# Kernel tuning notes

Hardware: AMD Instinct MI355X
Metric: run time of the kernel (lower is better)

Reference implementation:

```python
import jax, jax.numpy as jnp
import numpy as np

B, S, D, H = 2, 2048, 1024, 16
HEAD_DIM = D // H  # 64


def setup_inputs() -> dict:
    key = jax.random.key(0)
    ks = jax.random.split(key, 7)
    x = jax.random.normal(ks[0], (B, S, D), dtype=jnp.float32)
    W_q = jax.random.normal(ks[1], (D, D), dtype=jnp.float32) * 0.02
    W_k = jax.random.normal(ks[2], (D, D), dtype=jnp.float32) * 0.02
    W_v = jax.random.normal(ks[3], (D, D), dtype=jnp.float32) * 0.02
    W_o = jax.random.normal(ks[4], (D, D), dtype=jnp.float32) * 0.02 / np.sqrt(2 * 12)
    b_o = jnp.zeros((D,), dtype=jnp.float32)
    # Ragged prefix attention_mask: per-row valid lengths in [S/2, S];
    # row 0 forced to full length so max_valid_len == S statically (jit-safe).
    lengths = jax.random.randint(ks[5], (B,), S // 2, S + 1)
    lengths = lengths.at[0].set(S)
    attention_mask = (jnp.arange(S)[None, :] < lengths[:, None]).astype(jnp.float32)
    return {"x": x, "attention_mask": attention_mask, "W_q": W_q, "W_k": W_k,
            "W_v": W_v, "W_o": W_o, "b_o": b_o}


def reference(x, attention_mask, W_q, W_k, W_v, W_o, b_o):
    b, s, d = x.shape
    h, hd = H, HEAD_DIM
    # QKV projections (no bias, qkv_bias=False)
    q = (x @ W_q.T).reshape(b, s, h, hd).transpose(0, 2, 1, 3)  # [b,h,s,hd]
    # Masking keys/values at invalid (padded) positions; for prefix masks this
    # is exactly the module's per-batch packing loop (max_valid_len == s).
    m = attention_mask[:, None, :, None]  # [b,1,s,1]
    k = ((x @ W_k.T).reshape(b, s, h, hd).transpose(0, 2, 1, 3)) * m
    v = ((x @ W_v.T).reshape(b, s, h, hd).transpose(0, 2, 1, 3)) * m
    # Naive causal attention, same op order as the torch module:
    # mask with -inf first, then scale by 1/sqrt(head_dim), then softmax.
    causal = jnp.triu(jnp.ones((s, s), dtype=bool), 1)  # True above diagonal
    scores = jnp.einsum('bhqd,bhkd->bhqk', q, k)
    scores = jnp.where(causal[None, None], -jnp.inf, scores)
    att = jax.nn.softmax(scores / jnp.sqrt(jnp.float32(hd)), axis=-1)
    ctx = jnp.einsum('bhqk,bhkd->bhqd', att, v)  # [b,h,s,hd]
    ctx = ctx.transpose(0, 2, 1, 3).reshape(b, s, d)
    # Output projection (dropout is inference no-op)
    return ctx @ W_o.T + b_o
```

## Files before the change

kernel.cpp:

```cpp
#include <hip/hip_runtime.h>

#define B_  2
#define S_  2048
#define D_  1024
#define H_  16
#define HD_ 64
#define N3_ 3072
#define M_  4096

typedef _Float16 f16;
typedef _Float16 f16x2 __attribute__((ext_vector_type(2)));
typedef _Float16 f16x4 __attribute__((ext_vector_type(4)));
typedef _Float16 f16x8 __attribute__((ext_vector_type(8)));
typedef float    f32x4 __attribute__((ext_vector_type(4)));

__device__ __forceinline__ void async16(const f16* g, f16* l) {
  __builtin_amdgcn_global_load_lds(
      (const __attribute__((address_space(1))) unsigned int*)g,
      (__attribute__((address_space(3))) unsigned int*)l, 16, 0, 0);
}

__device__ __forceinline__ f16x2 pkrtz(float a, float b) {
  return __builtin_bit_cast(f16x2, __builtin_amdgcn_cvt_pkrtz(a, b));
}

__global__ __launch_bounds__(256)
void cvt_all(const float* __restrict__ x,
             const float* __restrict__ Wq, const float* __restrict__ Wk,
             const float* __restrict__ Wv, const float* __restrict__ Wo,
             f16* __restrict__ xb, f16* __restrict__ wdst, float qscale) {
  const int i = blockIdx.x * 256 + threadIdx.x;
  const int XN4 = M_ * D_ / 4;
  const int WN4 = D_ * D_ / 4;
  const float* src;
  f16* dst;
  float scale = 1.0f;
  int j;
  if (i < XN4) {
    src = x; dst = xb; j = i;
  } else {
    int k = i - XN4;
    int m = k >> 18;
    j = k & (WN4 - 1);
    src = (m == 0) ? Wq : (m == 1) ? Wk : (m == 2) ? Wv : Wo;
    if (m == 0) scale = qscale;
    dst = wdst + (size_t)m * D_ * D_;
  }
  float4 v = ((const float4*)src)[j];
  f16x4 o = { (f16)(v.x * scale), (f16)(v.y * scale),
              (f16)(v.z * scale), (f16)(v.w * scale) };
  ((f16x4*)dst)[j] = o;
}

__global__ __launch_bounds__(256)
void gemm_qkv(const f16* __restrict__ A, const f16* __restrict__ Bw,
              f16* __restrict__ Cq, f16* __restrict__ vtout,
              const float* __restrict__ mask) {
  __shared__ f16 As[128 * 64];
  __shared__ f16 Bs[128 * 64];

  const int tid  = threadIdx.x;
  const int lane = tid & 63;
  const int w    = tid >> 6;
  const int lcol = lane & 15;
  const int quad = lane >> 4;
  const int lx   = lcol & 7;
  const int wave_m = w >> 1, wave_n = w & 1;

  const int m0 = blockIdx.y * 128;
  const int n0 = blockIdx.x * 128;

  const int rr  = lane >> 3;
  const int gch = (lane & 7) ^ rr;

  const f16* gA[4];
  const f16* gB[4];
  f16* lA[4];
  f16* lB[4];
#pragma unroll
  for (int i = 0; i < 4; i++) {
    int seg = i * 4 + w;
    int row = seg * 8 + rr;
    gA[i] = A  + (size_t)(m0 + row) * D_ + gch * 8;
    gB[i] = Bw + (size_t)(n0 + row) * D_ + gch * 8;
    lA[i] = As + seg * 512;
    lB[i] = Bs + seg * 512;
  }

  int offA[4], offB[4];
#pragma unroll
  for (int i = 0; i < 4; i++) {
    offA[i] = (wave_m * 64 + i * 16 + lcol) * 64;
    offB[i] = (wave_n * 64 + i * 16 + lcol) * 64;
  }

  const f32x4 zero = {0.f, 0.f, 0.f, 0.f};
  f32x4 acc[4][4];
#pragma unroll
  for (int i = 0; i < 4; i++)
#pragma unroll
    for (int j = 0; j < 4; j++) acc[i][j] = zero;

  for (int k0 = 0; k0 < D_; k0 += 64) {
    __syncthreads();
#pragma unroll
    for (int i = 0; i < 4; i++) async16(gA[i] + k0, lA[i]);
#pragma unroll
    for (int i = 0; i < 4; i++) async16(gB[i] + k0, lB[i]);
    __syncthreads();

#pragma unroll
    for (int ks = 0; ks < 2; ks++) {
      const int co = ((quad + 4 * ks) ^ lx) * 8;
      f16x8 af[4], bf[4];
#pragma unroll
      for (int i = 0; i < 4; i++) af[i] = *(const f16x8*)(As + offA[i] + co);
#pragma unroll
      for (int i = 0; i < 4; i++) bf[i] = *(const f16x8*)(Bs + offB[i] + co);
#pragma unroll
      for (int mi = 0; mi < 4; mi++)
#pragma unroll
        for (int ni = 0; ni < 4; ni++)
          acc[mi][ni] = __builtin_amdgcn_mfma_f32_16x16x32_f16(
              af[mi], bf[ni], acc[mi][ni], 0, 0, 0);
    }
  }

  if (n0 >= 2 * D_) {
#pragma unroll
    for (int mi = 0; mi < 4; mi++) {
      const int mgb = m0 + wave_m * 64 + mi * 16 + quad * 4;
      const int b = mgb >> 11, s = mgb & (S_ - 1);
      const float mk0 = mask[mgb], mk1 = mask[mgb + 1];
      const float mk2 = mask[mgb + 2], mk3 = mask[mgb + 3];
#pragma unroll
      for (int ni = 0; ni < 4; ni++) {
        const int vcol = n0 - 2 * D_ + wave_n * 64 + ni * 16 + lcol;
        f16x4 v = { (f16)(acc[mi][ni][0] * mk0), (f16)(acc[mi][ni][1] * mk1),
                    (f16)(acc[mi][ni][2] * mk2), (f16)(acc[mi][ni][3] * mk3) };
        *(f16x4*)(vtout +
                  ((size_t)(b * 16 + (vcol >> 6)) * 64 + (vcol & 63)) * S_ + s) = v;
      }
    }
  } else {
    const bool kmask = (n0 >= D_);
#pragma unroll
    for (int mi = 0; mi < 4; mi++) {
#pragma unroll
      for (int r = 0; r < 4; r++) {
        int mg = m0 + wave_m * 64 + mi * 16 + quad * 4 + r;
        float mk = kmask ? mask[mg] : 1.0f;
#pragma unroll
        for (int ni = 0; ni < 4; ni++) {
          int ng = n0 + wave_n * 64 + ni * 16 + lcol;
          Cq[(size_t)mg * N3_ + ng] = (f16)(acc[mi][ni][r] * mk);
        }
      }
    }
  }
}

__global__ __launch_bounds__(256)
void gemm_proj(const f16* __restrict__ A, const f16* __restrict__ Bw,
               float* __restrict__ Cf, const float* __restrict__ bias) {
  __shared__ f16 As[64 * 64];
  __shared__ f16 Bs[128 * 64];

  const int tid  = threadIdx.x;
  const int lane = tid & 63;
  const int w    = tid >> 6;
  const int lcol = lane & 15;
  const int quad = lane >> 4;
  const int lx   = lcol & 7;
  const int wave_m = w >> 1, wave_n = w & 1;

  const int m0 = blockIdx.y * 64;
  const int n0 = blockIdx.x * 128;

  const int rr  = lane >> 3;
  const int gch = (lane & 7) ^ rr;

  const f16* gA[2];
  const f16* gB[4];
  f16* lA[2];
  f16* lB[4];
#pragma unroll
  for (int i = 0; i < 2; i++) {
    int seg = 2 * w + i;
    gA[i] = A + (size_t)(m0 + seg * 8 + rr) * D_ + gch * 8;
    lA[i] = As + seg * 512;
  }
#pragma unroll
  for (int i = 0; i < 4; i++) {
    int seg = i * 4 + w;
    gB[i] = Bw + (size_t)(n0 + seg * 8 + rr) * D_ + gch * 8;
    lB[i] = Bs + seg * 512;
  }

  int offA[2], offB[4];
#pragma unroll
  for (int i = 0; i < 2; i++) offA[i] = (wave_m * 32 + i * 16 + lcol) * 64;
#pragma unroll
  for (int i = 0; i < 4; i++) offB[i] = (wave_n * 64 + i * 16 + lcol) * 64;

  const f32x4 zero = {0.f, 0.f, 0.f, 0.f};
  f32x4 acc[2][4];
#pragma unroll
  for (int i = 0; i < 2; i++)
#pragma unroll
    for (int j = 0; j < 4; j++) acc[i][j] = zero;

  for (int k0 = 0; k0 < D_; k0 += 64) {
    __syncthreads();
#pragma unroll
    for (int i = 0; i < 2; i++) async16(gA[i] + k0, lA[i]);
#pragma unroll
    for (int i = 0; i < 4; i++) async16(gB[i] + k0, lB[i]);
    __syncthreads();

#pragma unroll
    for (int ks = 0; ks < 2; ks++) {
      const int co = ((quad + 4 * ks) ^ lx) * 8;
      f16x8 af[2], bf[4];
#pragma unroll
      for (int i = 0; i < 2; i++) af[i] = *(const f16x8*)(As + offA[i] + co);
#pragma unroll
      for (int i = 0; i < 4; i++) bf[i] = *(const f16x8*)(Bs + offB[i] + co);
#pragma unroll
      for (int mi = 0; mi < 2; mi++)
#pragma unroll
        for (int ni = 0; ni < 4; ni++)
          acc[mi][ni] = __builtin_amdgcn_mfma_f32_16x16x32_f16(
              af[mi], bf[ni], acc[mi][ni], 0, 0, 0);
    }
  }

#pragma unroll
  for (int mi = 0; mi < 2; mi++) {
#pragma unroll
    for (int r = 0; r < 4; r++) {
      int mg = m0 + wave_m * 32 + mi * 16 + quad * 4 + r;
#pragma unroll
      for (int ni = 0; ni < 4; ni++) {
        int ng = n0 + wave_n * 64 + ni * 16 + lcol;
        Cf[(size_t)mg * D_ + ng] = acc[mi][ni][r] + bias[ng];
      }
    }
  }
}

__global__ __launch_bounds__(256)
void flash_attn4(const f16* __restrict__ qkv, const f16* __restrict__ vt,
                 f16* __restrict__ ctx) {
  __shared__ f16 Ks[64 * 64];
  __shared__ f16 Vs[64 * 64];

  const int tid  = threadIdx.x;
  const int lane = tid & 63;
  const int w    = tid >> 6;
  const int lcol = lane & 15;
  const int quad = lane >> 4;
  const int lx   = lcol & 7;

  const int id   = blockIdx.x;
  const int bh   = (id & 7) + 8 * ((id >> 3) & 3);
  const int pair = id >> 5;
  const int b    = bh >> 4, h = bh & 15;
  const int qtA  = 31 - pair;
  const int qtB  = pair;

  const int rsub = lane >> 3;
  const int gch  = (lane & 7) ^ rsub;
  const int krow0 = w * 8 + rsub;
  const int krow1 = 32 + w * 8 + rsub;
  const f16* Kg = qkv + (size_t)b * S_ * N3_ + D_ + h * HD_;
  const f16* Vg = vt + (size_t)bh * HD_ * S_;
  f16* ldsK0 = Ks + (w * 8) * 64;
  f16* ldsK1 = Ks + (32 + w * 8) * 64;
  f16* ldsV0 = Vs + (w * 8) * 64;
  f16* ldsV1 = Vs + (32 + w * 8) * 64;

  const f32x4 zero = {0.f, 0.f, 0.f, 0.f};

  const int qrowA = qtA * 64 + w * 16 + lcol;
  const int qrowB = qtB * 64 + w * 16 + lcol;
  const f16* QpA = qkv + (size_t)(b * S_ + qrowA) * N3_ + h * HD_;
  const f16* QpB = qkv + (size_t)(b * S_ + qrowB) * N3_ + h * HD_;
  const f16x8 qbA0 = *(const f16x8*)(QpA + quad * 8);
  const f16x8 qbA1 = *(const f16x8*)(QpA + 32 + quad * 8);
  const f16x8 qbB0 = *(const f16x8*)(QpB + quad * 8);
  const f16x8 qbB1 = *(const f16x8*)(QpB + 32 + quad * 8);

  f32x4 oA[4], oB[4];
  float lpA = 0.f, lpB = 0.f;
#pragma unroll
  for (int i = 0; i < 4; i++) { oA[i] = zero; oB[i] = zero; }

  auto mask_diag = [&](f32x4* sc) {
#pragma unroll
    for (int ct = 0; ct < 4; ct++) {
      int koff = ct * 16 + quad * 4;
      int qoff = w * 16 + lcol;
#pragma unroll
      for (int r = 0; r < 4; r++)
        if (koff + r > qoff) sc[ct][r] = -1e30f;
    }
  };
  auto softmax_tiles = [&](f32x4* sc, f16x4* pf, float& lp) {
#pragma unroll
    for (int ct = 0; ct < 4; ct++) {
      float e0 = exp2f(sc[ct][0]);
      float e1 = exp2f(sc[ct][1]);
      float e2 = exp2f(sc[ct][2]);
      float e3 = exp2f(sc[ct][3]);
      lp += (e0 + e1) + (e2 + e3);
      f16x2 lo = pkrtz(e0, e1);
      f16x2 hi = pkrtz(e2, e3);
      f16x4 p = { lo[0], lo[1], hi[0], hi[1] };
      pf[ct] = p;
    }
  };

  for (int kt = 0; kt <= qtA; kt++) {
    const int kbase = kt * 64;
    __syncthreads();
    async16(Kg + (size_t)(kbase + krow0) * N3_ + gch * 8, ldsK0);
    async16(Kg + (size_t)(kbase + krow1) * N3_ + gch * 8, ldsK1);
    async16(Vg + (size_t)krow0 * S_ + kbase + gch * 8, ldsV0);
    async16(Vg + (size_t)krow1 * S_ + kbase + gch * 8, ldsV1);
    __syncthreads();

    const bool doB = (kt <= qtB);

    f16x8 kf0[4], kf1[4];
    f32x4 scA[4], scB[4];
#pragma unroll
    for (int ct = 0; ct < 4; ct++) {
      const f16* kr = Ks + (ct * 16 + lcol) * 64;
      kf0[ct] = *(const f16x8*)(kr + ((quad    ) ^ lx) * 8);
      kf1[ct] = *(const f16x8*)(kr + ((quad + 4) ^ lx) * 8);
      f32x4 z = zero;
      z = __builtin_amdgcn_mfma_f32_16x16x32_f16(kf0[ct], qbA0, z, 0, 0, 0);
      z = __builtin_amdgcn_mfma_f32_16x16x32_f16(kf1[ct], qbA1, z, 0, 0, 0);
      scA[ct] = z;
    }
    if (doB) {
#pragma unroll
      for (int ct = 0; ct < 4; ct++) {
        f32x4 z = zero;
        z = __builtin_amdgcn_mfma_f32_16x16x32_f16(kf0[ct], qbB0, z, 0, 0, 0);
        z = __builtin_amdgcn_mfma_f32_16x16x32_f16(kf1[ct], qbB1, z, 0, 0, 0);
        scB[ct] = z;
      }
    }

    if (kt == qtA) mask_diag(scA);
    if (doB && kt == qtB) mask_diag(scB);

    f16x4 pfA[4], pfB[4];
    softmax_tiles(scA, pfA, lpA);
    if (doB) softmax_tiles(scB, pfB, lpB);

#pragma unroll
    for (int ht = 0; ht < 4; ht++) {
      const f16* vr = Vs + (ht * 16 + lcol) * 64 + (quad & 1) * 4;
      f16x4 vf[4];
#pragma unroll
      for (int ct = 0; ct < 4; ct++)
        vf[ct] = *(const f16x4*)(vr + (((2 * ct + (quad >> 1)) ^ lx) * 8));
#pragma unroll
      for (int ct = 0; ct < 4; ct++)
        oA[ht] = __builtin_amdgcn_mfma_f32_16x16x16f16(vf[ct], pfA[ct], oA[ht], 0, 0, 0);
      if (doB) {
#pragma unroll
        for (int ct = 0; ct < 4; ct++)
          oB[ht] = __builtin_amdgcn_mfma_f32_16x16x16f16(vf[ct], pfB[ct], oB[ht], 0, 0, 0);
      }
    }
  }

  lpA += __shfl_xor(lpA, 16);
  lpA += __shfl_xor(lpA, 32);
  lpB += __shfl_xor(lpB, 16);
  lpB += __shfl_xor(lpB, 32);
  const float invA = 1.f / lpA;
  const float invB = 1.f / lpB;
  f16* cpA = ctx + (size_t)(b * S_ + qrowA) * D_ + h * HD_ + quad * 4;
  f16* cpB = ctx + (size_t)(b * S_ + qrowB) * D_ + h * HD_ + quad * 4;
#pragma unroll
  for (int ht = 0; ht < 4; ht++) {
    f16x4 ovA = { (f16)(oA[ht][0] * invA), (f16)(oA[ht][1] * invA),
                  (f16)(oA[ht][2] * invA), (f16)(oA[ht][3] * invA) };
    *(f16x4*)(cpA + ht * 16) = ovA;
    f16x4 ovB = { (f16)(oB[ht][0] * invB), (f16)(oB[ht][1] * invB),
                  (f16)(oB[ht][2] * invB), (f16)(oB[ht][3] * invB) };
    *(f16x4*)(cpB + ht * 16) = ovB;
  }
}

extern "C" void kernel_launch(void* const* d_in, const int* in_sizes, int n_in,
                              void* d_out, int out_size, void* d_ws, size_t ws_size,
                              hipStream_t stream) {
  (void)in_sizes; (void)n_in; (void)out_size; (void)ws_size;
  const float* x  = (const float*)d_in[0];
  const float* am = (const float*)d_in[1];
  const float* Wq = (const float*)d_in[2];
  const float* Wk = (const float*)d_in[3];
  const float* Wv = (const float*)d_in[4];
  const float* Wo = (const float*)d_in[5];
  const float* bo = (const float*)d_in[6];
  float* out = (float*)d_out;

  f16* ws   = (f16*)d_ws;
  f16* wqkv = ws;
  f16* wo16 = wqkv + (size_t)3 * D_ * D_;
  f16* xb   = wo16 + (size_t)D_ * D_;
  f16* qkvb = xb + (size_t)M_ * D_;
  f16* vtb  = qkvb + (size_t)M_ * N3_;
  f16* ctxb = vtb + (size_t)M_ * D_;

  const float qscale = 0.125f * 1.4426950408889634f;

  cvt_all<<<dim3((M_ * D_ + 4 * D_ * D_) / 1024), 256, 0, stream>>>(
      x, Wq, Wk, Wv, Wo, xb, wqkv, qscale);

  gemm_qkv<<<dim3(N3_ / 128, M_ / 128), 256, 0, stream>>>(
      xb, wqkv, qkvb, vtb, am);
  flash_attn4<<<dim3(512), 256, 0, stream>>>(qkvb, vtb, ctxb);
  gemm_proj<<<dim3(D_ / 128, M_ / 64), 256, 0, stream>>>(
      ctxb, wo16, out, bo);
}
```

Measured before the change: 186.5 us.

## Split paired query tiles into one tile per block with heavy-first ordering

The attention kernel no longer pairs a long and a short causal query tile per block and gives each block a single query tile, doubling the grid to 1024 blocks. Block IDs are ordered so the longest tiles are dispatched first, which keeps load balanced without pairing. This gives more blocks and lower register pressure per block for better occupancy. In exchange, K/V tiles that a pair used to share for both queries are now loaded into LDS twice, and there are more barriers.

```diff
diff --git a/kernel.cpp b/kernel.cpp
--- a/kernel.cpp
+++ b/kernel.cpp
@@ -250,7 +250,7 @@
 }
 
 __global__ __launch_bounds__(256)
-void flash_attn4(const f16* __restrict__ qkv, const f16* __restrict__ vt,
+void flash_attn5(const f16* __restrict__ qkv, const f16* __restrict__ vt,
                  f16* __restrict__ ctx) {
   __shared__ f16 Ks[64 * 64];
   __shared__ f16 Vs[64 * 64];
@@ -262,12 +262,15 @@
   const int quad = lane >> 4;
   const int lx   = lcol & 7;
 
-  const int id   = blockIdx.x;
-  const int bh   = (id & 7) + 8 * ((id >> 3) & 3);
-  const int pair = id >> 5;
-  const int b    = bh >> 4, h = bh & 15;
-  const int qtA  = 31 - pair;
-  const int qtB  = pair;
+  const int id = blockIdx.x;
+  const int bh = (id & 7) + 8 * ((id >> 3) & 3);
+  const int u  = id >> 5;
+  const int ua = u >> 3, ur = u & 7;
+  const int qt = (ua == 0) ? 31 - ur
+               : (ua == 1) ? 16 + ur
+               : (ua == 2) ? 15 - ur
+               : ur;
+  const int b = bh >> 4, h = bh & 15;
 
   const int rsub = lane >> 3;
   const int gch  = (lane & 7) ^ rsub;
@@ -282,31 +285,49 @@
 
   const f32x4 zero = {0.f, 0.f, 0.f, 0.f};
 
-  const int qrowA = qtA * 64 + w * 16 + lcol;
-  const int qrowB = qtB * 64 + w * 16 + lcol;
-  const f16* QpA = qkv + (size_t)(b * S_ + qrowA) * N3_ + h * HD_;
-  const f16* QpB = qkv + (size_t)(b * S_ + qrowB) * N3_ + h * HD_;
-  const f16x8 qbA0 = *(const f16x8*)(QpA + quad * 8);
-  const f16x8 qbA1 = *(const f16x8*)(QpA + 32 + quad * 8);
-  const f16x8 qbB0 = *(const f16x8*)(QpB + quad * 8);
-  const f16x8 qbB1 = *(const f16x8*)(QpB + 32 + quad * 8);
-
-  f32x4 oA[4], oB[4];
-  float lpA = 0.f, lpB = 0.f;
-#pragma unroll
-  for (int i = 0; i < 4; i++) { oA[i] = zero; oB[i] = zero; }
-
-  auto mask_diag = [&](f32x4* sc) {
+  const int qrow = qt * 64 + w * 16 + lcol;
+  const f16* Qp = qkv + (size_t)(b * S_ + qrow) * N3_ + h * HD_;
+  const f16x8 qb0 = *(const f16x8*)(Qp + quad * 8);
+  const f16x8 qb1 = *(const f16x8*)(Qp + 32 + quad * 8);
+
+  f32x4 o[4];
+  float lp = 0.f;
+#pragma unroll
+  for (int i = 0; i < 4; i++) o[i] = zero;
+
+  for (int kt = 0; kt <= qt; kt++) {
+    const int kbase = kt * 64;
+    __syncthreads();
+    async16(Kg + (size_t)(kbase + krow0) * N3_ + gch * 8, ldsK0);
+    async16(Kg + (size_t)(kbase + krow1) * N3_ + gch * 8, ldsK1);
+    async16(Vg + (size_t)krow0 * S_ + kbase + gch * 8, ldsV0);
+    async16(Vg + (size_t)krow1 * S_ + kbase + gch * 8, ldsV1);
+    __syncthreads();
+
+    f32x4 sc[4];
 #pragma unroll
     for (int ct = 0; ct < 4; ct++) {
-      int koff = ct * 16 + quad * 4;
-      int qoff = w * 16 + lcol;
-#pragma unroll
-      for (int r = 0; r < 4; r++)
-        if (koff + r > qoff) sc[ct][r] = -1e30f;
-    }
-  };
-  auto softmax_tiles = [&](f32x4* sc, f16x4* pf, float& lp) {
+      const f16* kr = Ks + (ct * 16 + lcol) * 64;
+      f16x8 kf0 = *(const f16x8*)(kr + ((quad    ) ^ lx) * 8);
+      f16x8 kf1 = *(const f16x8*)(kr + ((quad + 4) ^ lx) * 8);
+      f32x4 z = zero;
+      z = __builtin_amdgcn_mfma_f32_16x16x32_f16(kf0, qb0, z, 0, 0, 0);
+      z = __builtin_amdgcn_mfma_f32_16x16x32_f16(kf1, qb1, z, 0, 0, 0);
+      sc[ct] = z;
+    }
+
+    if (kt == qt) {
+#pragma unroll
+      for (int ct = 0; ct < 4; ct++) {
+        int koff = ct * 16 + quad * 4;
+        int qoff = w * 16 + lcol;
+#pragma unroll
+        for (int r = 0; r < 4; r++)
+          if (koff + r > qoff) sc[ct][r] = -1e30f;
+      }
+    }
+
+    f16x4 pf[4];
 #pragma unroll
     for (int ct = 0; ct < 4; ct++) {
       float e0 = exp2f(sc[ct][0]);
@@ -319,82 +340,27 @@
       f16x4 p = { lo[0], lo[1], hi[0], hi[1] };
       pf[ct] = p;
     }
-  };
-
-  for (int kt = 0; kt <= qtA; kt++) {
-    const int kbase = kt * 64;
-    __syncthreads();
-    async16(Kg + (size_t)(kbase + krow0) * N3_ + gch * 8, ldsK0);
-    async16(Kg + (size_t)(kbase + krow1) * N3_ + gch * 8, ldsK1);
-    async16(Vg + (size_t)krow0 * S_ + kbase + gch * 8, ldsV0);
-    async16(Vg + (size_t)krow1 * S_ + kbase + gch * 8, ldsV1);
-    __syncthreads();
-
-    const bool doB = (kt <= qtB);
-
-    f16x8 kf0[4], kf1[4];
-    f32x4 scA[4], scB[4];
-#pragma unroll
-    for (int ct = 0; ct < 4; ct++) {
-      const f16* kr = Ks + (ct * 16 + lcol) * 64;
-      kf0[ct] = *(const f16x8*)(kr + ((quad    ) ^ lx) * 8);
-      kf1[ct] = *(const f16x8*)(kr + ((quad + 4) ^ lx) * 8);
-      f32x4 z = zero;
-      z = __builtin_amdgcn_mfma_f32_16x16x32_f16(kf0[ct], qbA0, z, 0, 0, 0);
-      z = __builtin_amdgcn_mfma_f32_16x16x32_f16(kf1[ct], qbA1, z, 0, 0, 0);
-      scA[ct] = z;
-    }
-    if (doB) {
-#pragma unroll
-      for (int ct = 0; ct < 4; ct++) {
-        f32x4 z = zero;
-        z = __builtin_amdgcn_mfma_f32_16x16x32_f16(kf0[ct], qbB0, z, 0, 0, 0);
-        z = __builtin_amdgcn_mfma_f32_16x16x32_f16(kf1[ct], qbB1, z, 0, 0, 0);
-        scB[ct] = z;
-      }
-    }
-
-    if (kt == qtA) mask_diag(scA);
-    if (doB && kt == qtB) mask_diag(scB);
-
-    f16x4 pfA[4], pfB[4];
-    softmax_tiles(scA, pfA, lpA);
-    if (doB) softmax_tiles(scB, pfB, lpB);
 
 #pragma unroll
     for (int ht = 0; ht < 4; ht++) {
       const f16* vr = Vs + (ht * 16 + lcol) * 64 + (quad & 1) * 4;
-      f16x4 vf[4];
-#pragma unroll
-      for (int ct = 0; ct < 4; ct++)
-        vf[ct] = *(const f16x4*)(vr + (((2 * ct + (quad >> 1)) ^ lx) * 8));
-#pragma unroll
-      for (int ct = 0; ct < 4; ct++)
-        oA[ht] = __builtin_amdgcn_mfma_f32_16x16x16f16(vf[ct], pfA[ct], oA[ht], 0, 0, 0);
-      if (doB) {
-#pragma unroll
-        for (int ct = 0; ct < 4; ct++)
-          oB[ht] = __builtin_amdgcn_mfma_f32_16x16x16f16(vf[ct], pfB[ct], oB[ht], 0, 0, 0);
-      }
-    }
-  }
-
-  lpA += __shfl_xor(lpA, 16);
-  lpA += __shfl_xor(lpA, 32);
-  lpB += __shfl_xor(lpB, 16);
-  lpB += __shfl_xor(lpB, 32);
-  const float invA = 1.f / lpA;
-  const float invB = 1.f / lpB;
-  f16* cpA = ctx + (size_t)(b * S_ + qrowA) * D_ + h * HD_ + quad * 4;
-  f16* cpB = ctx + (size_t)(b * S_ + qrowB) * D_ + h * HD_ + quad * 4;
+#pragma unroll
+      for (int ct = 0; ct < 4; ct++) {
+        f16x4 vf = *(const f16x4*)(vr + (((2 * ct + (quad >> 1)) ^ lx) * 8));
+        o[ht] = __builtin_amdgcn_mfma_f32_16x16x16f16(vf, pf[ct], o[ht], 0, 0, 0);
+      }
+    }
+  }
+
+  lp += __shfl_xor(lp, 16);
+  lp += __shfl_xor(lp, 32);
+  const float inv = 1.f / lp;
+  f16* cp = ctx + (size_t)(b * S_ + qrow) * D_ + h * HD_ + quad * 4;
 #pragma unroll
   for (int ht = 0; ht < 4; ht++) {
-    f16x4 ovA = { (f16)(oA[ht][0] * invA), (f16)(oA[ht][1] * invA),
-                  (f16)(oA[ht][2] * invA), (f16)(oA[ht][3] * invA) };
-    *(f16x4*)(cpA + ht * 16) = ovA;
-    f16x4 ovB = { (f16)(oB[ht][0] * invB), (f16)(oB[ht][1] * invB),
-                  (f16)(oB[ht][2] * invB), (f16)(oB[ht][3] * invB) };
-    *(f16x4*)(cpB + ht * 16) = ovB;
+    f16x4 ov = { (f16)(o[ht][0] * inv), (f16)(o[ht][1] * inv),
+                 (f16)(o[ht][2] * inv), (f16)(o[ht][3] * inv) };
+    *(f16x4*)(cp + ht * 16) = ov;
   }
 }
 
@@ -426,7 +392,7 @@
 
   gemm_qkv<<<dim3(N3_ / 128, M_ / 128), 256, 0, stream>>>(
       xb, wqkv, qkvb, vtb, am);
-  flash_attn4<<<dim3(512), 256, 0, stream>>>(qkvb, vtb, ctxb);
+  flash_attn5<<<dim3(1024), 256, 0, stream>>>(qkvb, vtb, ctxb);
   gemm_proj<<<dim3(D_ / 128, M_ / 64), 256, 0, stream>>>(
       ctxb, wo16, out, bo);
 }
```

After: 184.2 us. Within noise of the previous version (-1.3%).
